# Kernel tuning notes

Hardware: AMD Instinct MI355X
Metric: run time of the kernel (lower is better)

Reference implementation:

```python
import jax, jax.numpy as jnp
import numpy as np

N, E, C_IN, H, K = 16384, 524288, 128, 64, 64


def setup_inputs() -> dict:
    key = jax.random.key(0)
    ks = jax.random.split(key, 6)
    x = jax.random.normal(ks[0], (N, C_IN), dtype=jnp.float32)
    edge_index = jax.random.randint(ks[1], (2, E), 0, N, dtype=jnp.int32)
    edge_weight = jax.random.uniform(ks[2], (E,), dtype=jnp.float32)
    sc = lambda f: 1.0 / np.sqrt(f)
    # GCNConv lin (no bias inside lin; separate bias), Glorot-ish init
    W1 = jax.random.normal(ks[3], (C_IN, H), dtype=jnp.float32) * sc(C_IN)
    b1 = jnp.zeros((H,), jnp.float32)
    # DMoNPooling MLP: Linear(H,H) then Linear(H,K), no activation between (act=None)
    Wm1 = jax.random.normal(ks[4], (H, H), dtype=jnp.float32) * sc(H)
    bm1 = jnp.zeros((H,), jnp.float32)
    Wm2 = jax.random.normal(ks[5], (H, K), dtype=jnp.float32) * sc(H)
    bm2 = jnp.zeros((K,), jnp.float32)
    return dict(x=x, edge_index=edge_index, edge_weight=edge_weight,
                W1=W1, b1=b1, Wm1=Wm1, bm1=bm1, Wm2=Wm2, bm2=bm2)


def gcn_conv(x, edge_index, edge_weight, W, b, n):
    # GCNConv: add self-loops (weight 1), symmetric deg^-1/2 normalization,
    # aggregate messages from source (row) into target (col).
    row, col = edge_index[0], edge_index[1]
    loop = jnp.arange(n, dtype=edge_index.dtype)
    row = jnp.concatenate([row, loop])
    col = jnp.concatenate([col, loop])
    w = jnp.concatenate([edge_weight, jnp.ones((n,), edge_weight.dtype)])
    deg = jax.ops.segment_sum(w, col, num_segments=n)
    dis = jnp.where(deg > 0, jax.lax.rsqrt(deg), 0.0)
    norm = dis[row] * w * dis[col]
    xw = x @ W  # [N, H]
    out = jax.ops.segment_sum(xw[row] * norm[:, None], col, num_segments=n)
    return out + b


def dmon_pool(h, adj, Wm1, bm1, Wm2, bm2):
    # eval mode: dropout disabled
    s = jax.nn.softmax((h @ Wm1 + bm1) @ Wm2 + bm2, axis=-1)  # [N, K]
    k = s.shape[-1]
    out_adj = s.T @ (adj @ s)  # [K, K]

    # Spectral (modularity) loss; degrees = einsum('ijk->ik', adj) = column sums
    deg = adj.sum(axis=0)  # [N]
    m = deg.sum() / 2
    ca = s.T @ deg  # [K], equals degrees^T s as well (symmetric roles)
    normalizer = jnp.outer(ca, ca) / 2 / m
    spectral_loss = -jnp.trace(out_adj - normalizer) / 2 / m

    # Orthogonality loss
    ss = s.T @ s  # [K, K]
    ss_fro = jnp.sqrt(jnp.sum(ss * ss))
    i_fro = jnp.sqrt(jnp.float32(k))  # ||I_K||_F
    diff = ss / ss_fro - jnp.eye(k, dtype=ss.dtype) / i_fro
    ortho_loss = jnp.sqrt(jnp.sum(diff * diff))

    # Cluster size loss
    cluster_size = s.sum(axis=0)  # [K]
    cluster_loss = jnp.sqrt(jnp.sum(cluster_size * cluster_size)) / h.shape[0] * i_fro - 1.0

    return s, spectral_loss, ortho_loss, cluster_loss


def reference(x, edge_index, edge_weight, W1, b1, Wm1, bm1, Wm2, bm2):
    h = jax.nn.relu(gcn_conv(x, edge_index, edge_weight, W1, b1, N))
    # to_dense_adj(edge_index): dense [N, N], duplicate edges summed
    adj = jnp.zeros((N, N), h.dtype).at[edge_index[0], edge_index[1]].add(1.0)
    s, spec, ortho, clus = dmon_pool(h, adj, Wm1, bm1, Wm2, bm2)
    return s[None], spec + ortho + clus
```

## Files before the change

kernel.cpp:

```cpp
#include <hip/hip_runtime.h>
#include <hip/hip_bf16.h>

typedef float          f4  __attribute__((ext_vector_type(4)));
typedef unsigned short us4 __attribute__((ext_vector_type(4)));
typedef int            i2  __attribute__((ext_vector_type(2)));

template <typename T>
__device__ __forceinline__ T ntload(const T* p) { return __builtin_nontemporal_load(p); }

__device__ __forceinline__ unsigned short f2bf(float f) {
    unsigned u = __float_as_uint(f);
    return (unsigned short)((u + 0x7FFF + ((u >> 16) & 1)) >> 16);
}
__device__ __forceinline__ float bf2f(unsigned short h) {
    return __uint_as_float((unsigned)h << 16);
}

__global__ __launch_bounds__(256) void k_degxw(const int* __restrict__ ei,
                      const float* __restrict__ ew,
                      unsigned* __restrict__ deg_rep,
                      const float* __restrict__ x, const float* __restrict__ W1,
                      float* __restrict__ xw, unsigned short* __restrict__ xw16,
                      int N, int E) {
    __shared__ float w1l[128 * 64];
    __shared__ f4    xt[16][32];
    if (blockIdx.x < 2048) {
        int e = blockIdx.x * 256 + threadIdx.x;
        if (e < E) {
            int c = ntload(ei + E + e);
            float w = ntload(ew + e);
            unsigned q = __float2uint_rn(w * 524288.f);
            atomicAdd(&deg_rep[(size_t)(blockIdx.x & 7) * N + c], (1u << 25) | q);
        }
        return;
    }
    int xbid = blockIdx.x - 2048;
    for (int t = threadIdx.x; t < 128 * 64; t += 256) w1l[t] = W1[t];
    int lane = threadIdx.x & 63;
    int wv   = threadIdx.x >> 6;
    for (int base = xbid * 16; base < N; base += 512 * 16) {
        __syncthreads();
        for (int t = threadIdx.x; t < 16 * 32; t += 256)
            ((f4*)xt)[t] = ntload((const f4*)x + (size_t)base * 32 + t);
        __syncthreads();
        int r0 = wv * 4;
        float a0 = 0.f, a1 = 0.f, a2 = 0.f, a3 = 0.f;
#pragma unroll
        for (int q = 0; q < 32; ++q) {
            f4 x0 = xt[r0][q], x1 = xt[r0 + 1][q], x2 = xt[r0 + 2][q], x3 = xt[r0 + 3][q];
            float wa = w1l[(4 * q + 0) * 64 + lane];
            float wb = w1l[(4 * q + 1) * 64 + lane];
            float wc = w1l[(4 * q + 2) * 64 + lane];
            float wd = w1l[(4 * q + 3) * 64 + lane];
            a0 = fmaf(x0.x, wa, a0); a0 = fmaf(x0.y, wb, a0); a0 = fmaf(x0.z, wc, a0); a0 = fmaf(x0.w, wd, a0);
            a1 = fmaf(x1.x, wa, a1); a1 = fmaf(x1.y, wb, a1); a1 = fmaf(x1.z, wc, a1); a1 = fmaf(x1.w, wd, a1);
            a2 = fmaf(x2.x, wa, a2); a2 = fmaf(x2.y, wb, a2); a2 = fmaf(x2.z, wc, a2); a2 = fmaf(x2.w, wd, a2);
            a3 = fmaf(x3.x, wa, a3); a3 = fmaf(x3.y, wb, a3); a3 = fmaf(x3.z, wc, a3); a3 = fmaf(x3.w, wd, a3);
        }
        int gr = base + r0;
        __builtin_nontemporal_store(a0, xw + (size_t)(gr + 0) * 64 + lane);
        __builtin_nontemporal_store(a1, xw + (size_t)(gr + 1) * 64 + lane);
        __builtin_nontemporal_store(a2, xw + (size_t)(gr + 2) * 64 + lane);
        __builtin_nontemporal_store(a3, xw + (size_t)(gr + 3) * 64 + lane);
        xw16[(size_t)(gr + 0) * 64 + lane] = f2bf(a0);
        xw16[(size_t)(gr + 1) * 64 + lane] = f2bf(a1);
        xw16[(size_t)(gr + 2) * 64 + lane] = f2bf(a2);
        xw16[(size_t)(gr + 3) * 64 + lane] = f2bf(a3);
    }
}

__global__ void k_red(const unsigned* __restrict__ deg_rep,
                      int* __restrict__ off_rep, int* __restrict__ cnt,
                      float* __restrict__ dis, int N) {
    int c = blockIdx.x * blockDim.x + threadIdx.x;
    if (c >= N) return;
    int run = 0;
    unsigned wsum = 0;
#pragma unroll
    for (int rep = 0; rep < 8; ++rep) {
        unsigned p = deg_rep[(size_t)rep * N + c];
        off_rep[(size_t)rep * N + c] = run;
        run += (int)(p >> 25);
        wsum += (p & ((1u << 25) - 1));
    }
    cnt[c] = run;
    dis[c] = rsqrtf((float)wsum * (1.f / 524288.f) + 1.0f);
}

__global__ void k_scan(const int* __restrict__ cnt, int* __restrict__ offs, int N) {
    __shared__ int wsum[16];
    int tid = threadIdx.x;
    int lane = tid & 63, wv = tid >> 6;
    int base = tid * 16;
    int loc[16];
    int sum = 0;
#pragma unroll
    for (int i = 0; i < 16; ++i) { loc[i] = sum; sum += cnt[base + i]; }
    int s = sum;
#pragma unroll
    for (int o = 1; o < 64; o <<= 1) {
        int t = __shfl_up(s, o);
        if (lane >= o) s += t;
    }
    if (lane == 63) wsum[wv] = s;
    __syncthreads();
    if (wv == 0 && lane < 16) {
        int ws = wsum[lane];
        int ss = ws;
#pragma unroll
        for (int o = 1; o < 16; o <<= 1) {
            int t = __shfl_up(ss, o);
            if (lane >= o) ss += t;
        }
        wsum[lane] = ss - ws;
    }
    __syncthreads();
    int excl = s - sum + wsum[wv];
#pragma unroll
    for (int i = 0; i < 16; ++i) offs[base + i] = excl + loc[i];
    if (tid == 1023) offs[N] = excl + sum;
}

__global__ void k_bucket(const int* __restrict__ ei, const float* __restrict__ ew,
                         const float* __restrict__ dis, const int* __restrict__ offs,
                         const int* __restrict__ off_rep, int* __restrict__ cursor_rep,
                         i2* __restrict__ barr, int N, int E) {
    int e = blockIdx.x * blockDim.x + threadIdx.x;
    if (e < E) {
        int rep = blockIdx.x & 7;
        int r = ntload(ei + e), c = ntload(ei + E + e);
        float norm = dis[r] * ntload(ew + e) * dis[c];
        size_t rc = (size_t)rep * N + c;
        int pos = offs[c] + off_rep[rc] + atomicAdd(&cursor_rep[rc], 1);
        i2 rec; rec.x = r; rec.y = __float_as_int(norm);
        barr[pos] = rec;
    }
}

__global__ __launch_bounds__(512) void k_gmlp(const int* __restrict__ offs,
                         const i2* __restrict__ barr,
                         const float* __restrict__ xw, const unsigned short* __restrict__ xw16,
                         const float* __restrict__ dis, const float* __restrict__ b1,
                         const float* __restrict__ Wm1, const float* __restrict__ bm1,
                         const float* __restrict__ Wm2, const float* __restrict__ bm2,
                         float* __restrict__ s, unsigned short* __restrict__ s16, int N) {
    __shared__ float w1m[4096], w2m[4096];
    __shared__ float hsc[8][2][64];
    __shared__ float tsc[8][2][64];
    for (int t = threadIdx.x; t < 4096; t += 512) { w1m[t] = Wm1[t]; w2m[t] = Wm2[t]; }
    __syncthreads();
    int lane = threadIdx.x & 63;
    int sub = lane >> 4, q = lane & 15;
    int wv   = threadIdx.x >> 6;
    int wid  = blockIdx.x * 8 + wv;
    int nw   = 8 * gridDim.x;
    const us4* xw16v = (const us4*)xw16;
    for (int cp = wid; cp < (N >> 1); cp += nw) {
        int c0 = 2 * cp, c1 = c0 + 1;
        int beg = ntload(offs + c0), mid = ntload(offs + c1), end = ntload(offs + c1 + 1);
        f4 A0 = {0.f, 0.f, 0.f, 0.f}, A1 = A0, B0 = A0, B1 = A0;
        int i = beg;
        i2 bcur = (beg + lane < end) ? ntload(barr + beg + lane) : (i2){0, 0};
        while (i < end) {
            int inext = i + 64;
            i2 bnxt = {0, 0};
            if (inext + lane < end) bnxt = ntload(barr + inext + lane);
            int nloc = min(64, end - i);
            int   rv = bcur.x;
            float nv = __int_as_float(bcur.y);
            int jmax = (nloc + 3) >> 2;
            int j = 0;
            for (; j + 4 <= jmax; j += 4) {
                int e0 = 4 * j + sub;
                int g0 = i + e0;
                int   r0 = __shfl(rv, e0),      r1 = __shfl(rv, e0 + 4);
                int   r2 = __shfl(rv, e0 + 8),  r3 = __shfl(rv, e0 + 12);
                float n0 = __shfl(nv, e0),      n1 = __shfl(nv, e0 + 4);
                float n2 = __shfl(nv, e0 + 8),  n3 = __shfl(nv, e0 + 12);
                us4 u0 = xw16v[(size_t)r0 * 16 + q];
                us4 u1 = xw16v[(size_t)r1 * 16 + q];
                us4 u2 = xw16v[(size_t)r2 * 16 + q];
                us4 u3 = xw16v[(size_t)r3 * 16 + q];
                float a0w = (g0      < mid) ? n0 : 0.f, b0w = n0 - a0w;
                float a1w = (g0 + 4  < mid) ? n1 : 0.f, b1w = n1 - a1w;
                float a2w = (g0 + 8  < mid) ? n2 : 0.f, b2w = n2 - a2w;
                float a3w = (g0 + 12 < mid) ? n3 : 0.f, b3w = n3 - a3w;
                A0.x = fmaf(bf2f(u0.x), a0w, A0.x); A0.y = fmaf(bf2f(u0.y), a0w, A0.y);
                A0.z = fmaf(bf2f(u0.z), a0w, A0.z); A0.w = fmaf(bf2f(u0.w), a0w, A0.w);
                B0.x = fmaf(bf2f(u0.x), b0w, B0.x); B0.y = fmaf(bf2f(u0.y), b0w, B0.y);
                B0.z = fmaf(bf2f(u0.z), b0w, B0.z); B0.w = fmaf(bf2f(u0.w), b0w, B0.w);
                A1.x = fmaf(bf2f(u1.x), a1w, A1.x); A1.y = fmaf(bf2f(u1.y), a1w, A1.y);
                A1.z = fmaf(bf2f(u1.z), a1w, A1.z); A1.w = fmaf(bf2f(u1.w), a1w, A1.w);
                B1.x = fmaf(bf2f(u1.x), b1w, B1.x); B1.y = fmaf(bf2f(u1.y), b1w, B1.y);
                B1.z = fmaf(bf2f(u1.z), b1w, B1.z); B1.w = fmaf(bf2f(u1.w), b1w, B1.w);
                A0.x = fmaf(bf2f(u2.x), a2w, A0.x); A0.y = fmaf(bf2f(u2.y), a2w, A0.y);
                A0.z = fmaf(bf2f(u2.z), a2w, A0.z); A0.w = fmaf(bf2f(u2.w), a2w, A0.w);
                B0.x = fmaf(bf2f(u2.x), b2w, B0.x); B0.y = fmaf(bf2f(u2.y), b2w, B0.y);
                B0.z = fmaf(bf2f(u2.z), b2w, B0.z); B0.w = fmaf(bf2f(u2.w), b2w, B0.w);
                A1.x = fmaf(bf2f(u3.x), a3w, A1.x); A1.y = fmaf(bf2f(u3.y), a3w, A1.y);
                A1.z = fmaf(bf2f(u3.z), a3w, A1.z); A1.w = fmaf(bf2f(u3.w), a3w, A1.w);
                B1.x = fmaf(bf2f(u3.x), b3w, B1.x); B1.y = fmaf(bf2f(u3.y), b3w, B1.y);
                B1.z = fmaf(bf2f(u3.z), b3w, B1.z); B1.w = fmaf(bf2f(u3.w), b3w, B1.w);
            }
            for (; j < jmax; ++j) {
                int e = 4 * j + sub;
                int g = i + e;
                int   r  = __shfl(rv, e);
                float nm = __shfl(nv, e);
                us4 u = xw16v[(size_t)r * 16 + q];
                float aw = (g < mid) ? nm : 0.f, bw = nm - aw;
                A0.x = fmaf(bf2f(u.x), aw, A0.x); A0.y = fmaf(bf2f(u.y), aw, A0.y);
                A0.z = fmaf(bf2f(u.z), aw, A0.z); A0.w = fmaf(bf2f(u.w), aw, A0.w);
                B0.x = fmaf(bf2f(u.x), bw, B0.x); B0.y = fmaf(bf2f(u.y), bw, B0.y);
                B0.z = fmaf(bf2f(u.z), bw, B0.z); B0.w = fmaf(bf2f(u.w), bw, B0.w);
            }
            i = inext;
            bcur = bnxt;
        }
        A0.x += A1.x; A0.y += A1.y; A0.z += A1.z; A0.w += A1.w;
        B0.x += B1.x; B0.y += B1.y; B0.z += B1.z; B0.w += B1.w;
        A0.x += __shfl_xor(A0.x, 16); A0.y += __shfl_xor(A0.y, 16);
        A0.z += __shfl_xor(A0.z, 16); A0.w += __shfl_xor(A0.w, 16);
        B0.x += __shfl_xor(B0.x, 16); B0.y += __shfl_xor(B0.y, 16);
        B0.z += __shfl_xor(B0.z, 16); B0.w += __shfl_xor(B0.w, 16);
        A0.x += __shfl_xor(A0.x, 32); A0.y += __shfl_xor(A0.y, 32);
        A0.z += __shfl_xor(A0.z, 32); A0.w += __shfl_xor(A0.w, 32);
        B0.x += __shfl_xor(B0.x, 32); B0.y += __shfl_xor(B0.y, 32);
        B0.z += __shfl_xor(B0.z, 32); B0.w += __shfl_xor(B0.w, 32);
        f4 bb = ((const f4*)b1)[q];
        f4 self0 = ntload((const f4*)xw + (size_t)c0 * 16 + q);
        f4 self1 = ntload((const f4*)xw + (size_t)c1 * 16 + q);
        float d0 = dis[c0], d1 = dis[c1];
        float dd0 = d0 * d0, dd1 = d1 * d1;
        f4 v0, v1;
        v0.x = A0.x + self0.x * dd0 + bb.x; v0.y = A0.y + self0.y * dd0 + bb.y;
        v0.z = A0.z + self0.z * dd0 + bb.z; v0.w = A0.w + self0.w * dd0 + bb.w;
        v1.x = B0.x + self1.x * dd1 + bb.x; v1.y = B0.y + self1.y * dd1 + bb.y;
        v1.z = B0.z + self1.z * dd1 + bb.z; v1.w = B0.w + self1.w * dd1 + bb.w;
        v0.x = v0.x > 0.f ? v0.x : 0.f; v0.y = v0.y > 0.f ? v0.y : 0.f;
        v0.z = v0.z > 0.f ? v0.z : 0.f; v0.w = v0.w > 0.f ? v0.w : 0.f;
        v1.x = v1.x > 0.f ? v1.x : 0.f; v1.y = v1.y > 0.f ? v1.y : 0.f;
        v1.z = v1.z > 0.f ? v1.z : 0.f; v1.w = v1.w > 0.f ? v1.w : 0.f;
        if (sub == 0) {
            ((f4*)hsc[wv][0])[q] = v0;
            ((f4*)hsc[wv][1])[q] = v1;
        }
        float t0 = bm1[lane], t1 = t0;
#pragma unroll
        for (int k = 0; k < 16; ++k) {
            f4 ha = ((f4*)hsc[wv][0])[k];
            f4 hb = ((f4*)hsc[wv][1])[k];
            float wa = w1m[(4 * k + 0) * 64 + lane];
            float wb = w1m[(4 * k + 1) * 64 + lane];
            float wc = w1m[(4 * k + 2) * 64 + lane];
            float wd = w1m[(4 * k + 3) * 64 + lane];
            t0 = fmaf(ha.x, wa, t0); t0 = fmaf(ha.y, wb, t0);
            t0 = fmaf(ha.z, wc, t0); t0 = fmaf(ha.w, wd, t0);
            t1 = fmaf(hb.x, wa, t1); t1 = fmaf(hb.y, wb, t1);
            t1 = fmaf(hb.z, wc, t1); t1 = fmaf(hb.w, wd, t1);
        }
        tsc[wv][0][lane] = t0;
        tsc[wv][1][lane] = t1;
        float g0 = bm2[lane], g1 = g0;
#pragma unroll
        for (int k = 0; k < 16; ++k) {
            f4 ta = ((f4*)tsc[wv][0])[k];
            f4 tb = ((f4*)tsc[wv][1])[k];
            float wa = w2m[(4 * k + 0) * 64 + lane];
            float wb = w2m[(4 * k + 1) * 64 + lane];
            float wc = w2m[(4 * k + 2) * 64 + lane];
            float wd = w2m[(4 * k + 3) * 64 + lane];
            g0 = fmaf(ta.x, wa, g0); g0 = fmaf(ta.y, wb, g0);
            g0 = fmaf(ta.z, wc, g0); g0 = fmaf(ta.w, wd, g0);
            g1 = fmaf(tb.x, wa, g1); g1 = fmaf(tb.y, wb, g1);
            g1 = fmaf(tb.z, wc, g1); g1 = fmaf(tb.w, wd, g1);
        }
        float m0 = g0, m1 = g1;
#pragma unroll
        for (int o = 32; o > 0; o >>= 1) {
            m0 = fmaxf(m0, __shfl_xor(m0, o));
            m1 = fmaxf(m1, __shfl_xor(m1, o));
        }
        float e0 = __expf(g0 - m0), e1 = __expf(g1 - m1);
        float z0 = e0, z1 = e1;
#pragma unroll
        for (int o = 32; o > 0; o >>= 1) {
            z0 += __shfl_xor(z0, o);
            z1 += __shfl_xor(z1, o);
        }
        float o0 = e0 / z0, o1 = e1 / z1;
        __builtin_nontemporal_store(o0, s + (size_t)c0 * 64 + lane);
        __builtin_nontemporal_store(o1, s + (size_t)c1 * 64 + lane);
        s16[(size_t)c0 * 64 + lane] = f2bf(o0);
        s16[(size_t)c1 * 64 + lane] = f2bf(o1);
    }
}

__global__ __launch_bounds__(256) void k_rt(const int* __restrict__ offs,
                         const i2* __restrict__ barr,
                         const unsigned short* __restrict__ s16,
                         const float* __restrict__ s, const int* __restrict__ cnt,
                         float* __restrict__ ssg, float* __restrict__ cag,
                         float* __restrict__ csg, float* __restrict__ tracearr, int N) {
    __shared__ float tile[64][64];
    __shared__ float bsum;
    int lane = threadIdx.x & 63;
    int wv   = threadIdx.x >> 6;
    if (blockIdx.x >= 2048) {
        int base = (blockIdx.x - 2048) * 64;
        if (base >= N) return;
        for (int t = threadIdx.x; t < 1024; t += 256)
            ((f4*)tile)[t] = ntload((const f4*)(s + (size_t)base * 64) + t);
        __syncthreads();
        float acc[16];
#pragma unroll
        for (int i = 0; i < 16; ++i) acc[i] = 0.f;
        for (int r = 0; r < 64; ++r) {
            float sj = tile[r][lane];
            const float* brow = &tile[r][wv * 16];
#pragma unroll
            for (int i = 0; i < 16; ++i) acc[i] = fmaf(brow[i], sj, acc[i]);
        }
        float csj = 0.f, caj = 0.f;
#pragma unroll
        for (int i = 0; i < 16; ++i) {
            int r = wv * 16 + i;
            float sj = tile[r][lane];
            csj += sj;
            caj = fmaf(sj, (float)cnt[base + r], caj);
        }
#pragma unroll
        for (int i = 0; i < 16; ++i) atomicAdd(&ssg[(wv * 16 + i) * 64 + lane], acc[i]);
        atomicAdd(&csg[lane], csj);
        atomicAdd(&cag[lane], caj);
        return;
    }
    int sub = lane >> 4, q = lane & 15;
    int wid  = blockIdx.x * 4 + wv;
    int nw   = 4 * 2048;
    const us4* s16v = (const us4*)s16;
    float tacc = 0.f;
    for (int cp = wid; cp < (N >> 1); cp += nw) {
        int c0 = 2 * cp, c1 = c0 + 1;
        int beg = ntload(offs + c0), mid = ntload(offs + c1), end = ntload(offs + c1 + 1);
        us4 scu0 = s16v[(size_t)c0 * 16 + q];
        us4 scu1 = s16v[(size_t)c1 * 16 + q];
        f4 sc0 = {bf2f(scu0.x), bf2f(scu0.y), bf2f(scu0.z), bf2f(scu0.w)};
        f4 sc1 = {bf2f(scu1.x), bf2f(scu1.y), bf2f(scu1.z), bf2f(scu1.w)};
        f4 A0 = {0.f, 0.f, 0.f, 0.f}, A1 = A0, B0 = A0, B1 = A0;
        int i = beg;
        int rcur = (beg + lane < end) ? ntload(barr + beg + lane).x : 0;
        while (i < end) {
            int inext = i + 64;
            int rnxt = 0;
            if (inext + lane < end) rnxt = ntload(barr + inext + lane).x;
            int nloc = min(64, end - i);
            int rv = rcur;
            int jmax = (nloc + 3) >> 2;
            int j = 0;
            for (; j + 4 <= jmax; j += 4) {
                int e0 = 4 * j + sub;
                int g0 = i + e0;
                int r0 = __shfl(rv, e0),     r1 = __shfl(rv, e0 + 4);
                int r2 = __shfl(rv, e0 + 8), r3 = __shfl(rv, e0 + 12);
                float n0 = (e0      < nloc) ? 1.f : 0.f;
                float n1 = (e0 + 4  < nloc) ? 1.f : 0.f;
                float n2 = (e0 + 8  < nloc) ? 1.f : 0.f;
                float n3 = (e0 + 12 < nloc) ? 1.f : 0.f;
                us4 u0 = s16v[(size_t)r0 * 16 + q];
                us4 u1 = s16v[(size_t)r1 * 16 + q];
                us4 u2 = s16v[(size_t)r2 * 16 + q];
                us4 u3 = s16v[(size_t)r3 * 16 + q];
                float a0w = (g0      < mid) ? n0 : 0.f, b0w = n0 - a0w;
                float a1w = (g0 + 4  < mid) ? n1 : 0.f, b1w = n1 - a1w;
                float a2w = (g0 + 8  < mid) ? n2 : 0.f, b2w = n2 - a2w;
                float a3w = (g0 + 12 < mid) ? n3 : 0.f, b3w = n3 - a3w;
                A0.x = fmaf(bf2f(u0.x), a0w, A0.x); A0.y = fmaf(bf2f(u0.y), a0w, A0.y);
                A0.z = fmaf(bf2f(u0.z), a0w, A0.z); A0.w = fmaf(bf2f(u0.w), a0w, A0.w);
                B0.x = fmaf(bf2f(u0.x), b0w, B0.x); B0.y = fmaf(bf2f(u0.y), b0w, B0.y);
                B0.z = fmaf(bf2f(u0.z), b0w, B0.z); B0.w = fmaf(bf2f(u0.w), b0w, B0.w);
                A1.x = fmaf(bf2f(u1.x), a1w, A1.x); A1.y = fmaf(bf2f(u1.y), a1w, A1.y);
                A1.z = fmaf(bf2f(u1.z), a1w, A1.z); A1.w = fmaf(bf2f(u1.w), a1w, A1.w);
                B1.x = fmaf(bf2f(u1.x), b1w, B1.x); B1.y = fmaf(bf2f(u1.y), b1w, B1.y);
                B1.z = fmaf(bf2f(u1.z), b1w, B1.z); B1.w = fmaf(bf2f(u1.w), b1w, B1.w);
                A0.x = fmaf(bf2f(u2.x), a2w, A0.x); A0.y = fmaf(bf2f(u2.y), a2w, A0.y);
                A0.z = fmaf(bf2f(u2.z), a2w, A0.z); A0.w = fmaf(bf2f(u2.w), a2w, A0.w);
                B0.x = fmaf(bf2f(u2.x), b2w, B0.x); B0.y = fmaf(bf2f(u2.y), b2w, B0.y);
                B0.z = fmaf(bf2f(u2.z), b2w, B0.z); B0.w = fmaf(bf2f(u2.w), b2w, B0.w);
                A1.x = fmaf(bf2f(u3.x), a3w, A1.x); A1.y = fmaf(bf2f(u3.y), a3w, A1.y);
                A1.z = fmaf(bf2f(u3.z), a3w, A1.z); A1.w = fmaf(bf2f(u3.w), a3w, A1.w);
                B1.x = fmaf(bf2f(u3.x), b3w, B1.x); B1.y = fmaf(bf2f(u3.y), b3w, B1.y);
                B1.z = fmaf(bf2f(u3.z), b3w, B1.z); B1.w = fmaf(bf2f(u3.w), b3w, B1.w);
            }
            for (; j < jmax; ++j) {
                int e = 4 * j + sub;
                int g = i + e;
                int r = __shfl(rv, e);
                float m = (e < nloc) ? 1.f : 0.f;
                us4 u = s16v[(size_t)r * 16 + q];
                float aw = (g < mid) ? m : 0.f, bw = m - aw;
                A0.x = fmaf(bf2f(u.x), aw, A0.x); A0.y = fmaf(bf2f(u.y), aw, A0.y);
                A0.z = fmaf(bf2f(u.z), aw, A0.z); A0.w = fmaf(bf2f(u.w), aw, A0.w);
                B0.x = fmaf(bf2f(u.x), bw, B0.x); B0.y = fmaf(bf2f(u.y), bw, B0.y);
                B0.z = fmaf(bf2f(u.z), bw, B0.z); B0.w = fmaf(bf2f(u.w), bw, B0.w);
            }
            i = inext;
            rcur = rnxt;
        }
        A0.x += A1.x; A0.y += A1.y; A0.z += A1.z; A0.w += A1.w;
        B0.x += B1.x; B0.y += B1.y; B0.z += B1.z; B0.w += B1.w;
        A0.x += __shfl_xor(A0.x, 16); A0.y += __shfl_xor(A0.y, 16);
        A0.z += __shfl_xor(A0.z, 16); A0.w += __shfl_xor(A0.w, 16);
        B0.x += __shfl_xor(B0.x, 16); B0.y += __shfl_xor(B0.y, 16);
        B0.z += __shfl_xor(B0.z, 16); B0.w += __shfl_xor(B0.w, 16);
        A0.x += __shfl_xor(A0.x, 32); A0.y += __shfl_xor(A0.y, 32);
        A0.z += __shfl_xor(A0.z, 32); A0.w += __shfl_xor(A0.w, 32);
        B0.x += __shfl_xor(B0.x, 32); B0.y += __shfl_xor(B0.y, 32);
        B0.z += __shfl_xor(B0.z, 32); B0.w += __shfl_xor(B0.w, 32);
        tacc += A0.x * sc0.x + A0.y * sc0.y + A0.z * sc0.z + A0.w * sc0.w;
        tacc += B0.x * sc1.x + B0.y * sc1.y + B0.z * sc1.z + B0.w * sc1.w;
    }
    tacc *= 0.25f;
#pragma unroll
    for (int o = 32; o > 0; o >>= 1) tacc += __shfl_xor(tacc, o);
    if (threadIdx.x == 0) bsum = 0.f;
    __syncthreads();
    if (lane == 0) atomicAdd(&bsum, tacc);
    __syncthreads();
    if (threadIdx.x == 0) tracearr[blockIdx.x] = bsum;
}

__global__ void k_final(const float* __restrict__ ssg, const float* __restrict__ cag,
                        const float* __restrict__ csg, const float* __restrict__ tracearr,
                        int ntr, float Ef, float Nf, float* __restrict__ out) {
    __shared__ float red[256];
    int tid = threadIdx.x;

    float a = 0.f;
    for (int t = tid; t < ntr; t += 256) a += tracearr[t];
    red[tid] = a; __syncthreads();
    for (int o = 128; o > 0; o >>= 1) { if (tid < o) red[tid] += red[tid + o]; __syncthreads(); }
    float trace = red[0]; __syncthreads();

    a = 0.f;
    for (int t = tid; t < 4096; t += 256) { float v = ssg[t]; a += v * v; }
    red[tid] = a; __syncthreads();
    for (int o = 128; o > 0; o >>= 1) { if (tid < o) red[tid] += red[tid + o]; __syncthreads(); }
    float ss_sumsq = red[0]; __syncthreads();

    a = (tid < 64) ? ssg[tid * 64 + tid] : 0.f;
    red[tid] = a; __syncthreads();
    for (int o = 128; o > 0; o >>= 1) { if (tid < o) red[tid] += red[tid + o]; __syncthreads(); }
    float tr_ss = red[0]; __syncthreads();

    a = (tid < 64) ? cag[tid] * cag[tid] : 0.f;
    red[tid] = a; __syncthreads();
    for (int o = 128; o > 0; o >>= 1) { if (tid < o) red[tid] += red[tid + o]; __syncthreads(); }
    float ca_ss = red[0]; __syncthreads();

    a = (tid < 64) ? csg[tid] * csg[tid] : 0.f;
    red[tid] = a; __syncthreads();
    for (int o = 128; o > 0; o >>= 1) { if (tid < o) red[tid] += red[tid + o]; __syncthreads(); }
    float cs_ss = red[0];

    if (tid == 0) {
        float spec = -(trace - ca_ss / Ef) / Ef;
        float ss_fro = sqrtf(ss_sumsq);
        float ortho = sqrtf(fmaxf(2.f - tr_ss / (4.f * ss_fro), 0.f));
        float clus = sqrtf(cs_ss) / Nf * 8.f - 1.f;
        out[0] = spec + ortho + clus;
    }
}

extern "C" void kernel_launch(void* const* d_in, const int* in_sizes, int n_in,
                              void* d_out, int out_size, void* d_ws, size_t ws_size,
                              hipStream_t stream) {
    const float* x   = (const float*)d_in[0];
    const int*   ei  = (const int*)d_in[1];
    const float* ew  = (const float*)d_in[2];
    const float* W1  = (const float*)d_in[3];
    const float* b1  = (const float*)d_in[4];
    const float* Wm1 = (const float*)d_in[5];
    const float* bm1 = (const float*)d_in[6];
    const float* Wm2 = (const float*)d_in[7];
    const float* bm2 = (const float*)d_in[8];

    const int N = in_sizes[0] / 128;
    const int E = in_sizes[2];
    const int TGRID = 2304;

    char* base = (char*)d_ws;
    unsigned* deg_rep = (unsigned*)base;
    int*   cursor_rep = (int*)(base + (size_t)32 * N);
    float* ssg = (float*)(base + (size_t)64 * N);
    float* cag = ssg + 4096;
    float* csg = cag + 64;
    size_t zbytes = (size_t)64 * N + (4096 + 128) * 4;
    char* up = base + ((zbytes + 15) & ~(size_t)15);
    int*   cnt = (int*)up;            up += (size_t)4 * N;
    float* dis = (float*)up;          up += (size_t)4 * N;
    int*   offs = (int*)up;           up += (size_t)4 * (N + 1);
    float* tracearr = (float*)up;     up += (size_t)4 * 2048;
    up = (char*)(((size_t)up + 15) & ~(size_t)15);
    float* xw = (float*)up;           up += (size_t)4 * N * 64;
    int*   off_rep = (int*)up;        up += (size_t)32 * N;
    i2*    barr = (i2*)up;            up += (size_t)8 * E;
    unsigned short* xw16 = (unsigned short*)up; up += (size_t)2 * N * 64;
    unsigned short* s16  = (unsigned short*)up;
    float* sbuf = (float*)d_out;

    hipMemsetAsync(d_ws, 0, zbytes, stream);

    k_degxw<<<2560, 256, 0, stream>>>(ei, ew, deg_rep, x, W1, xw, xw16, N, E);
    k_red<<<(N + 255) / 256, 256, 0, stream>>>(deg_rep, off_rep, cnt, dis, N);
    k_scan<<<1, 1024, 0, stream>>>(cnt, offs, N);
    k_bucket<<<(E + 255) / 256, 256, 0, stream>>>(ei, ew, dis, offs, off_rep, cursor_rep, barr, N, E);
    k_gmlp<<<1024, 512, 0, stream>>>(offs, barr, xw, xw16, dis, b1, Wm1, bm1, Wm2, bm2, sbuf, s16, N);
    k_rt<<<TGRID, 256, 0, stream>>>(offs, barr, s16, sbuf, cnt, ssg, cag, csg, tracearr, N);
    k_final<<<1, 256, 0, stream>>>(ssg, cag, csg, tracearr, 2048, (float)E, (float)N,
                                   ((float*)d_out) + (size_t)N * 64);
}
```

Before: 222.9 us.

## Merge bucket cursor and offsets, prefetch next node pair in gmlp, halve grid

k_red now writes the per-replica prefix offsets straight into the cursor array, so k_bucket does one atomicAdd per edge without a separate off_rep load and the memset shrinks. k_gmlp prefetches the next pair's offsets and first edge chunk while it does the reduction, MLP and softmax for the current pair, hiding gather latency across loop iterations. Its grid is also halved to 512 blocks, so each wave handles more pairs and the weight load into shared memory is amortised, at some cost in parallelism.

```diff
diff --git a/kernel.cpp b/kernel.cpp
--- a/kernel.cpp
+++ b/kernel.cpp
@@ -70,7 +70,7 @@
 }
 
 __global__ void k_red(const unsigned* __restrict__ deg_rep,
-                      int* __restrict__ off_rep, int* __restrict__ cnt,
+                      int* __restrict__ cursor_rep, int* __restrict__ cnt,
                       float* __restrict__ dis, int N) {
     int c = blockIdx.x * blockDim.x + threadIdx.x;
     if (c >= N) return;
@@ -79,7 +79,7 @@
 #pragma unroll
     for (int rep = 0; rep < 8; ++rep) {
         unsigned p = deg_rep[(size_t)rep * N + c];
-        off_rep[(size_t)rep * N + c] = run;
+        cursor_rep[(size_t)rep * N + c] = run;
         run += (int)(p >> 25);
         wsum += (p & ((1u << 25) - 1));
     }
@@ -123,15 +123,14 @@
 
 __global__ void k_bucket(const int* __restrict__ ei, const float* __restrict__ ew,
                          const float* __restrict__ dis, const int* __restrict__ offs,
-                         const int* __restrict__ off_rep, int* __restrict__ cursor_rep,
-                         i2* __restrict__ barr, int N, int E) {
+                         int* __restrict__ cursor_rep, i2* __restrict__ barr,
+                         int N, int E) {
     int e = blockIdx.x * blockDim.x + threadIdx.x;
     if (e < E) {
         int rep = blockIdx.x & 7;
         int r = ntload(ei + e), c = ntload(ei + E + e);
         float norm = dis[r] * ntload(ew + e) * dis[c];
-        size_t rc = (size_t)rep * N + c;
-        int pos = offs[c] + off_rep[rc] + atomicAdd(&cursor_rep[rc], 1);
+        int pos = offs[c] + atomicAdd(&cursor_rep[(size_t)rep * N + c], 1);
         i2 rec; rec.x = r; rec.y = __float_as_int(norm);
         barr[pos] = rec;
     }
@@ -152,15 +151,17 @@
     int lane = threadIdx.x & 63;
     int sub = lane >> 4, q = lane & 15;
     int wv   = threadIdx.x >> 6;
-    int wid  = blockIdx.x * 8 + wv;
+    int NP   = N >> 1;
     int nw   = 8 * gridDim.x;
+    int cp   = blockIdx.x * 8 + wv;
+    if (cp >= NP) return;
+    int c0 = 2 * cp, c1 = c0 + 1;
+    int beg = ntload(offs + c0), mid = ntload(offs + c1), end = ntload(offs + c1 + 1);
+    i2 bcur = (beg + lane < end) ? ntload(barr + beg + lane) : (i2){0, 0};
     const us4* xw16v = (const us4*)xw16;
-    for (int cp = wid; cp < (N >> 1); cp += nw) {
-        int c0 = 2 * cp, c1 = c0 + 1;
-        int beg = ntload(offs + c0), mid = ntload(offs + c1), end = ntload(offs + c1 + 1);
+    for (;;) {
         f4 A0 = {0.f, 0.f, 0.f, 0.f}, A1 = A0, B0 = A0, B1 = A0;
         int i = beg;
-        i2 bcur = (beg + lane < end) ? ntload(barr + beg + lane) : (i2){0, 0};
         while (i < end) {
             int inext = i + 64;
             i2 bnxt = {0, 0};
@@ -217,6 +218,13 @@
             i = inext;
             bcur = bnxt;
         }
+        int cpn = cp + nw;
+        int begN = 0, midN = 0, endN = 0;
+        if (cpn < NP) {
+            begN = ntload(offs + 2 * cpn);
+            midN = ntload(offs + 2 * cpn + 1);
+            endN = ntload(offs + 2 * cpn + 2);
+        }
         A0.x += A1.x; A0.y += A1.y; A0.z += A1.z; A0.w += A1.w;
         B0.x += B1.x; B0.y += B1.y; B0.z += B1.z; B0.w += B1.w;
         A0.x += __shfl_xor(A0.x, 16); A0.y += __shfl_xor(A0.y, 16);
@@ -227,6 +235,7 @@
         A0.z += __shfl_xor(A0.z, 32); A0.w += __shfl_xor(A0.w, 32);
         B0.x += __shfl_xor(B0.x, 32); B0.y += __shfl_xor(B0.y, 32);
         B0.z += __shfl_xor(B0.z, 32); B0.w += __shfl_xor(B0.w, 32);
+        if (cpn < NP) bcur = (begN + lane < endN) ? ntload(barr + begN + lane) : (i2){0, 0};
         f4 bb = ((const f4*)b1)[q];
         f4 self0 = ntload((const f4*)xw + (size_t)c0 * 16 + q);
         f4 self1 = ntload((const f4*)xw + (size_t)c1 * 16 + q);
@@ -293,6 +302,9 @@
         __builtin_nontemporal_store(o1, s + (size_t)c1 * 64 + lane);
         s16[(size_t)c0 * 64 + lane] = f2bf(o0);
         s16[(size_t)c1 * 64 + lane] = f2bf(o1);
+        if (cpn >= NP) break;
+        cp = cpn; c0 = 2 * cp; c1 = c0 + 1;
+        beg = begN; mid = midN; end = endN;
     }
 }
 
@@ -491,19 +503,18 @@
 
     char* base = (char*)d_ws;
     unsigned* deg_rep = (unsigned*)base;
-    int*   cursor_rep = (int*)(base + (size_t)32 * N);
-    float* ssg = (float*)(base + (size_t)64 * N);
+    float* ssg = (float*)(base + (size_t)32 * N);
     float* cag = ssg + 4096;
     float* csg = cag + 64;
-    size_t zbytes = (size_t)64 * N + (4096 + 128) * 4;
+    size_t zbytes = (size_t)32 * N + (4096 + 128) * 4;
     char* up = base + ((zbytes + 15) & ~(size_t)15);
+    int*   cursor_rep = (int*)up;     up += (size_t)32 * N;
     int*   cnt = (int*)up;            up += (size_t)4 * N;
     float* dis = (float*)up;          up += (size_t)4 * N;
     int*   offs = (int*)up;           up += (size_t)4 * (N + 1);
     float* tracearr = (float*)up;     up += (size_t)4 * 2048;
     up = (char*)(((size_t)up + 15) & ~(size_t)15);
     float* xw = (float*)up;           up += (size_t)4 * N * 64;
-    int*   off_rep = (int*)up;        up += (size_t)32 * N;
     i2*    barr = (i2*)up;            up += (size_t)8 * E;
     unsigned short* xw16 = (unsigned short*)up; up += (size_t)2 * N * 64;
     unsigned short* s16  = (unsigned short*)up;
@@ -512,10 +523,10 @@
     hipMemsetAsync(d_ws, 0, zbytes, stream);
 
     k_degxw<<<2560, 256, 0, stream>>>(ei, ew, deg_rep, x, W1, xw, xw16, N, E);
-    k_red<<<(N + 255) / 256, 256, 0, stream>>>(deg_rep, off_rep, cnt, dis, N);
+    k_red<<<(N + 255) / 256, 256, 0, stream>>>(deg_rep, cursor_rep, cnt, dis, N);
     k_scan<<<1, 1024, 0, stream>>>(cnt, offs, N);
-    k_bucket<<<(E + 255) / 256, 256, 0, stream>>>(ei, ew, dis, offs, off_rep, cursor_rep, barr, N, E);
-    k_gmlp<<<1024, 512, 0, stream>>>(offs, barr, xw, xw16, dis, b1, Wm1, bm1, Wm2, bm2, sbuf, s16, N);
+    k_bucket<<<(E + 255) / 256, 256, 0, stream>>>(ei, ew, dis, offs, cursor_rep, barr, N, E);
+    k_gmlp<<<512, 512, 0, stream>>>(offs, barr, xw, xw16, dis, b1, Wm1, bm1, Wm2, bm2, sbuf, s16, N);
     k_rt<<<TGRID, 256, 0, stream>>>(offs, barr, s16, sbuf, cnt, ssg, cag, csg, tracearr, N);
     k_final<<<1, 256, 0, stream>>>(ssg, cag, csg, tracearr, 2048, (float)E, (float)N,
                                    ((float*)d_out) + (size_t)N * 64);
```

Measured after the change: 220.0 us. Within noise of the previous version (-1.3%).
